# Optimization experiments

Measured on AMD Instinct MI355X. Metric: run time of the kernel, lower is better.

The kernel has to match this reference:

```python
import jax, jax.numpy as jnp
import numpy as np

N = 10000          # nodes
E = 80000          # edges
STATE_DIM = 18
HID = 1024
LAYERS = 4


def setup_inputs() -> dict:
    key = jax.random.key(0)
    ks = jax.random.split(key, 16)
    s = 0.02
    x = jax.random.normal(ks[0], (N, STATE_DIM), dtype=jnp.float32)
    edge_index = jax.random.randint(ks[1], (2, E), 0, N, dtype=jnp.int32)
    # frozen inverse-phase embedding projection (no bias)
    proj_w = jax.random.normal(ks[2], (STATE_DIM, HID), dtype=jnp.float32) * s
    # per-layer message MLP: Linear(2*HID -> HID) -> ReLU -> Linear(HID -> HID)
    W1 = jax.random.normal(ks[3], (LAYERS, 2 * HID, HID), dtype=jnp.float32) * s
    b1 = jnp.zeros((LAYERS, HID), dtype=jnp.float32)
    W2 = jax.random.normal(ks[4], (LAYERS, HID, HID), dtype=jnp.float32) * s
    b2 = jnp.zeros((LAYERS, HID), dtype=jnp.float32)
    # ghost head: Linear(HID->256) -> ReLU -> Linear(256->1) -> Sigmoid
    gw1 = jax.random.normal(ks[5], (HID, 256), dtype=jnp.float32) * s
    gb1 = jnp.zeros((256,), dtype=jnp.float32)
    gw2 = jax.random.normal(ks[6], (256, 1), dtype=jnp.float32) * s
    gb2 = jnp.zeros((1,), dtype=jnp.float32)
    # state head: Linear(HID -> STATE_DIM)
    sw = jax.random.normal(ks[7], (HID, STATE_DIM), dtype=jnp.float32) * s
    sb = jnp.zeros((STATE_DIM,), dtype=jnp.float32)
    return {"x": x, "edge_index": edge_index, "proj_w": proj_w,
            "W1": W1, "b1": b1, "W2": W2, "b2": b2,
            "gw1": gw1, "gb1": gb1, "gw2": gw2, "gb2": gb2,
            "sw": sw, "sb": sb}


def reference(x, edge_index, proj_w, W1, b1, W2, b2, gw1, gb1, gw2, gb2, sw, sb):
    src = edge_index[0]  # j (source)
    dst = edge_index[1]  # i (target), aggr='add' scatters into i
    # InversePhaseEmbedding: sin(h)*cos(h)
    p = x @ proj_w                      # [N, HID]
    h = jnp.sin(p) * jnp.cos(p)
    for l in range(LAYERS):
        x_i = h[dst]                    # [E, HID] gather target feats
        x_j = h[src]                    # [E, HID] gather source feats
        msg = jnp.concatenate([x_i, x_j - x_i], axis=-1)  # [E, 2*HID]
        m = jax.nn.relu(msg @ W1[l] + b1[l]) @ W2[l] + b2[l]  # [E, HID]
        h = jax.ops.segment_sum(m, dst, num_segments=N)       # scatter-add
        h = jax.nn.relu(h)
    ghost_score = jax.nn.sigmoid(jax.nn.relu(h @ gw1 + gb1) @ gw2 + gb2)  # [N,1]
    stable_state = h @ sw + sb                                            # [N,18]
    return ghost_score, stable_state, h
```

## Files before the change

kernel.cpp:

```cpp
#include <hip/hip_runtime.h>
#include <hip/hip_bf16.h>
#include <math.h>

#define NN 10000
#define EE 80000
#define SDIM 18
#define HID 1024
#define NLAYERS 4
#define GHID 256

typedef __bf16 bf16;
typedef __bf16 bf16x8 __attribute__((ext_vector_type(8)));
typedef __bf16 bf16x4 __attribute__((ext_vector_type(4)));
typedef float f32x4 __attribute__((ext_vector_type(4)));

#define AS1C(p) ((const __attribute__((address_space(1))) void*)(p))
#define AS3(p)  ((__attribute__((address_space(3))) void*)(p))

__global__ void count_kernel(const int* __restrict__ ei, int* __restrict__ cnt) {
    int e = blockIdx.x * 256 + threadIdx.x;
    if (e < EE) atomicAdd(&cnt[ei[EE + e]], 1);
}

__global__ __launch_bounds__(256) void scan_kernel(const int* __restrict__ cnt,
                                                   int* __restrict__ offs,
                                                   int* __restrict__ cursor,
                                                   float* __restrict__ degF) {
    const int CH = 40;
    __shared__ int partial[256];
    int t = threadIdx.x;
    int base = t * CH;
    int local[CH];
    int sum = 0;
#pragma unroll
    for (int i = 0; i < CH; ++i) {
        int idx = base + i;
        int v = (idx < NN) ? cnt[idx] : 0;
        local[i] = sum;
        sum += v;
    }
    partial[t] = sum;
    __syncthreads();
    for (int off = 1; off < 256; off <<= 1) {
        int v = (t >= off) ? partial[t - off] : 0;
        __syncthreads();
        partial[t] += v;
        __syncthreads();
    }
    int excl = (t == 0) ? 0 : partial[t - 1];
#pragma unroll
    for (int i = 0; i < CH; ++i) {
        int idx = base + i;
        if (idx < NN) {
            int o = excl + local[i];
            offs[idx] = o;
            cursor[idx] = o;
            degF[idx] = (float)cnt[idx];
        }
    }
    if (t == 255) offs[NN] = partial[255];
}

__global__ void scatter_kernel(const int* __restrict__ ei, int* __restrict__ cursor,
                               int* __restrict__ esrc) {
    int e = blockIdx.x * 256 + threadIdx.x;
    if (e < EE) {
        int dst = ei[EE + e];
        int pos = atomicAdd(&cursor[dst], 1);
        esrc[pos] = ei[e];
    }
}

__global__ __launch_bounds__(256) void prep_kernel(const float* __restrict__ W1,
                                                   const float* __restrict__ W2,
                                                   const float* __restrict__ gw1,
                                                   const float* __restrict__ sw,
                                                   const float* __restrict__ b1,
                                                   bf16* __restrict__ WT,
                                                   bf16* __restrict__ W2t,
                                                   bf16* __restrict__ gw1t,
                                                   bf16* __restrict__ swt,
                                                   float* __restrict__ cb,
                                                   int* __restrict__ cnt) {
    __shared__ float td[32][33];
    __shared__ float tb[32][33];
    const size_t H2 = (size_t)HID * HID;
    int b = blockIdx.x;
    int tx = threadIdx.x & 31, ty = threadIdx.x >> 5;

    if (b < 4096) {
        int l = b >> 10, r = b & 1023;
        int bx = (r & 31) * 32, by = (r >> 5) * 32;
        const float* s = W1 + (size_t)l * 2 * H2;
        bf16* d = WT + (size_t)l * 2 * H2;
#pragma unroll
        for (int r4 = 0; r4 < 4; ++r4) {
            int row = by + ty + r4 * 8;
            float vt = s[(size_t)row * HID + bx + tx];
            float vb = s[H2 + (size_t)row * HID + bx + tx];
            td[ty + r4 * 8][tx] = vt - vb;
            tb[ty + r4 * 8][tx] = vb;
        }
        __syncthreads();
#pragma unroll
        for (int r4 = 0; r4 < 4; ++r4) {
            int orow = bx + ty + r4 * 8;
            d[(size_t)orow * HID + by + tx] = (bf16)td[tx][ty + r4 * 8];
            d[(size_t)(HID + orow) * HID + by + tx] = (bf16)tb[tx][ty + r4 * 8];
        }
    } else if (b < 8192) {
        int sub = b - 4096;
        int l = sub >> 10, r = sub & 1023;
        int bx = (r & 31) * 32, by = (r >> 5) * 32;
        const float* s = W2 + (size_t)l * H2;
        bf16* d = W2t + (size_t)l * H2;
#pragma unroll
        for (int r4 = 0; r4 < 4; ++r4) {
            int row = by + ty + r4 * 8;
            td[ty + r4 * 8][tx] = s[(size_t)row * HID + bx + tx];
        }
        __syncthreads();
#pragma unroll
        for (int r4 = 0; r4 < 4; ++r4) {
            int orow = bx + ty + r4 * 8;
            d[(size_t)orow * HID + by + tx] = (bf16)td[tx][ty + r4 * 8];
        }
    } else if (b < 8448) {
        int sub = b - 8192;
        int bx = (sub & 7) * 32, by = (sub >> 3) * 32;
#pragma unroll
        for (int r4 = 0; r4 < 4; ++r4) {
            int row = by + ty + r4 * 8;
            td[ty + r4 * 8][tx] = gw1[(size_t)row * GHID + bx + tx];
        }
        __syncthreads();
#pragma unroll
        for (int r4 = 0; r4 < 4; ++r4) {
            int orow = bx + ty + r4 * 8;
            gw1t[(size_t)orow * HID + by + tx] = (bf16)td[tx][ty + r4 * 8];
        }
    } else if (b < 8576) {
        int i = (b - 8448) * 256 + threadIdx.x;
        int n = i >> 10, k = i & 1023;
        swt[i] = (bf16)(n < SDIM ? sw[k * SDIM + n] : 0.f);
    } else if (b < 8608) {
        int i = (b - 8576) * 256 + threadIdx.x;
        int l = i >> 11, c = i & 2047;
        cb[i] = (c < HID) ? b1[l * HID + c] : 0.f;
    } else {
        int i = (b - 8608) * 256 + threadIdx.x;
        if (i < NN) cnt[i] = 0;
    }
}

__global__ __launch_bounds__(256) void proj_kernel(const float* __restrict__ x,
                                                   const float* __restrict__ pw,
                                                   bf16* __restrict__ hb) {
    int row = blockIdx.y;
    int col = blockIdx.x * 256 + threadIdx.x;
    __shared__ float xr[SDIM];
    if (threadIdx.x < SDIM) xr[threadIdx.x] = x[row * SDIM + threadIdx.x];
    __syncthreads();
    float acc = 0.f;
#pragma unroll
    for (int k = 0; k < SDIM; ++k) acc += xr[k] * pw[k * HID + col];
    hb[(size_t)row * HID + col] = (bf16)(sinf(acc) * cosf(acc));
}

template <int RELU, int HAS_BIAS, int HAS_RS, int WF32, int WB16>
__global__ __launch_bounds__(256) void mgemm_kernel(const bf16* __restrict__ A,
                                                    const bf16* __restrict__ Bt,
                                                    float* __restrict__ C,
                                                    bf16* __restrict__ Cb,
                                                    const float* __restrict__ bias,
                                                    const float* __restrict__ rowscale,
                                                    int M, int N, int K) {
    __shared__ bf16 As[2][128 * 32];
    __shared__ bf16 Bs[2][128 * 32];
    const int tid = threadIdx.x;

    const int num_n = gridDim.x, num_m = gridDim.y;
    int bid = blockIdx.x + blockIdx.y * num_n;
    const int GROUP = 8;
    int width = GROUP * num_n;
    int group = bid / width;
    int rem = bid - group * width;
    int rows_ing = num_m - group * GROUP;
    rows_ing = rows_ing < GROUP ? rows_ing : GROUP;
    int by = group * GROUP + rem % rows_ing;
    int bx = rem / rows_ing;
    const int m0 = by * 128;
    const int n0 = bx * 128;

    const int wave = tid >> 6;
    const int wr = (wave >> 1) * 64, wc = (wave & 1) * 64;
    const int lane = tid & 63;
    const int quad = lane >> 4, r15 = lane & 15;

    f32x4 acc[4][4] = {};

    const int s0 = tid, s1 = 256 + tid;
    const int seg0 = ((s0 & 3) ^ ((s0 >> 3) & 3)) * 8;
    const int seg1 = ((s1 & 3) ^ ((s1 >> 3) & 3)) * 8;
    int ar0 = m0 + (s0 >> 2); ar0 = ar0 < M ? ar0 : M - 1;
    int ar1 = m0 + (s1 >> 2); ar1 = ar1 < M ? ar1 : M - 1;
    const bf16* ga0 = A + (size_t)ar0 * K + seg0;
    const bf16* ga1 = A + (size_t)ar1 * K + seg1;
    const bf16* gb0 = Bt + (size_t)(n0 + (s0 >> 2)) * K + seg0;
    const bf16* gb1 = Bt + (size_t)(n0 + (s1 >> 2)) * K + seg1;
    const int lofs0 = (tid & ~63) * 8;
    const int lofs1 = 2048 + (tid & ~63) * 8;

    int aoff[4], boff[4];
#pragma unroll
    for (int i = 0; i < 4; ++i) {
        int rA = wr + i * 16 + r15;
        aoff[i] = rA * 32 + (quad ^ ((rA >> 1) & 3)) * 8;
        int rB = wc + i * 16 + r15;
        boff[i] = rB * 32 + (quad ^ ((rB >> 1) & 3)) * 8;
    }

    __builtin_amdgcn_global_load_lds(AS1C(ga0), AS3(&As[0][lofs0]), 16, 0, 0);
    __builtin_amdgcn_global_load_lds(AS1C(ga1), AS3(&As[0][lofs1]), 16, 0, 0);
    __builtin_amdgcn_global_load_lds(AS1C(gb0), AS3(&Bs[0][lofs0]), 16, 0, 0);
    __builtin_amdgcn_global_load_lds(AS1C(gb1), AS3(&Bs[0][lofs1]), 16, 0, 0);

    const int NIT = K >> 5;
    for (int k = 0; k < NIT; ++k) {
        const int buf = k & 1;
        __syncthreads();
        if (k + 1 < NIT) {
            const int ko = (k + 1) << 5;
            __builtin_amdgcn_global_load_lds(AS1C(ga0 + ko), AS3(&As[buf ^ 1][lofs0]), 16, 0, 0);
            __builtin_amdgcn_global_load_lds(AS1C(ga1 + ko), AS3(&As[buf ^ 1][lofs1]), 16, 0, 0);
            __builtin_amdgcn_global_load_lds(AS1C(gb0 + ko), AS3(&Bs[buf ^ 1][lofs0]), 16, 0, 0);
            __builtin_amdgcn_global_load_lds(AS1C(gb1 + ko), AS3(&Bs[buf ^ 1][lofs1]), 16, 0, 0);
        }
        bf16x8 af[4], bfr[4];
#pragma unroll
        for (int i = 0; i < 4; ++i)
            af[i] = *(const bf16x8*)(&As[buf][aoff[i]]);
#pragma unroll
        for (int j = 0; j < 4; ++j)
            bfr[j] = *(const bf16x8*)(&Bs[buf][boff[j]]);
#pragma unroll
        for (int i = 0; i < 4; ++i)
#pragma unroll
            for (int j = 0; j < 4; ++j)
                acc[i][j] = __builtin_amdgcn_mfma_f32_16x16x32_bf16(af[i], bfr[j], acc[i][j], 0, 0, 0);
    }

#pragma unroll
    for (int i = 0; i < 4; ++i) {
#pragma unroll
        for (int r = 0; r < 4; ++r) {
            int grow = m0 + wr + i * 16 + quad * 4 + r;
            if (grow >= M) continue;
            float rs = HAS_RS ? rowscale[grow] : 1.f;
#pragma unroll
            for (int j = 0; j < 4; ++j) {
                int gcol = n0 + wc + j * 16 + r15;
                float v = acc[i][j][r];
                if (HAS_BIAS) v += rs * bias[gcol];
                if (RELU) v = fmaxf(v, 0.f);
                if (WF32) C[(size_t)grow * N + gcol] = v;
                if (WB16) Cb[(size_t)grow * N + gcol] = (bf16)v;
            }
        }
    }
}

__global__ __launch_bounds__(256) void gather_kernel(const int* __restrict__ offs,
                                                     const int* __restrict__ esrc,
                                                     const bf16* __restrict__ CB,
                                                     bf16* __restrict__ Sb) {
    int half = threadIdx.x >> 7;
    int t = threadIdx.x & 127;
    int node = blockIdx.x * 2 + half;
    int c = t * 8;
    int k0 = offs[node], k1 = offs[node + 1];
    bf16x8 cv = *(const bf16x8*)(CB + (size_t)node * 2048 + c);
    float cf[8], a[8];
#pragma unroll
    for (int i = 0; i < 8; ++i) { cf[i] = (float)cv[i]; a[i] = 0.f; }
    for (int k = k0; k < k1; ++k) {
        int s = esrc[k];
        bf16x8 bv = *(const bf16x8*)(CB + (size_t)s * 2048 + 1024 + c);
#pragma unroll
        for (int i = 0; i < 8; ++i) a[i] += fmaxf(cf[i] + (float)bv[i], 0.f);
    }
    bf16x8 o;
#pragma unroll
    for (int i = 0; i < 8; ++i) o[i] = (bf16)a[i];
    *(bf16x8*)(Sb + (size_t)node * HID + c) = o;
}

__global__ __launch_bounds__(64) void stable_mfma_kernel(const bf16* __restrict__ hb,
                                                         const bf16* __restrict__ swt,
                                                         const float* __restrict__ sb,
                                                         float* __restrict__ out) {
    int m0 = blockIdx.x * 16;
    int lane = threadIdx.x;
    int quad = lane >> 4, r15 = lane & 15;
    f32x4 acc0 = {}, acc1 = {};
    const bf16* arow = hb + (size_t)(m0 + r15) * HID + quad * 8;
    const bf16* b0 = swt + (size_t)r15 * HID + quad * 8;
    const bf16* b1p = swt + (size_t)(16 + r15) * HID + quad * 8;
    for (int k0 = 0; k0 < HID; k0 += 32) {
        bf16x8 af = *(const bf16x8*)(arow + k0);
        bf16x8 bf0 = *(const bf16x8*)(b0 + k0);
        bf16x8 bf1 = *(const bf16x8*)(b1p + k0);
        acc0 = __builtin_amdgcn_mfma_f32_16x16x32_bf16(af, bf0, acc0, 0, 0, 0);
        acc1 = __builtin_amdgcn_mfma_f32_16x16x32_bf16(af, bf1, acc1, 0, 0, 0);
    }
#pragma unroll
    for (int r = 0; r < 4; ++r) {
        int grow = m0 + quad * 4 + r;
        out[(size_t)grow * SDIM + r15] = acc0[r] + sb[r15];
        if (r15 < 2) out[(size_t)grow * SDIM + 16 + r15] = acc1[r] + sb[16 + r15];
    }
}

__global__ __launch_bounds__(256) void ghost_kernel(const float* __restrict__ g1,
                                                    const float* __restrict__ gw2,
                                                    const float* __restrict__ gb2,
                                                    float* __restrict__ out) {
    int w = threadIdx.x >> 6, lane = threadIdx.x & 63;
    int row = blockIdx.x * 4 + w;
    const float4 gv = *(const float4*)(g1 + (size_t)row * GHID + lane * 4);
    const float4 wv = *(const float4*)(gw2 + lane * 4);
    float v = gv.x * wv.x + gv.y * wv.y + gv.z * wv.z + gv.w * wv.w;
#pragma unroll
    for (int o = 32; o > 0; o >>= 1) v += __shfl_down(v, o, 64);
    if (lane == 0) out[row] = 1.f / (1.f + expf(-(v + gb2[0])));
}

extern "C" void kernel_launch(void* const* d_in, const int* in_sizes, int n_in,
                              void* d_out, int out_size, void* d_ws, size_t ws_size,
                              hipStream_t stream) {
    const float* x   = (const float*)d_in[0];
    const int*   ei  = (const int*)d_in[1];
    const float* pw  = (const float*)d_in[2];
    const float* W1  = (const float*)d_in[3];
    const float* b1  = (const float*)d_in[4];
    const float* W2  = (const float*)d_in[5];
    const float* b2  = (const float*)d_in[6];
    const float* gw1 = (const float*)d_in[7];
    const float* gb1 = (const float*)d_in[8];
    const float* gw2 = (const float*)d_in[9];
    const float* gb2 = (const float*)d_in[10];
    const float* sw  = (const float*)d_in[11];
    const float* sb  = (const float*)d_in[12];

    float* out    = (float*)d_out;
    float* ghost  = out;
    float* stable = out + NN;
    float* h      = out + NN + NN * SDIM;

    const size_t H2 = (size_t)HID * HID;
    float* ws   = (float*)d_ws;
    float* g1   = ws;
    float* degF = g1 + (size_t)NN * GHID;
    float* cb   = degF + NN;
    bf16* hb    = (bf16*)(cb + 4 * 2048);
    bf16* Sb    = hb + (size_t)NN * HID;
    bf16* CB    = Sb + (size_t)NN * HID;
    bf16* WT    = CB + (size_t)NN * 2048;
    bf16* W2t   = WT + 8 * H2;
    bf16* gw1t  = W2t + 4 * H2;
    bf16* swt   = gw1t + (size_t)GHID * HID;
    int*  cnt    = (int*)(swt + 32 * 1024);
    int*  offs   = cnt + NN;
    int*  cursor = offs + NN + 1;
    int*  esrc   = cursor + NN;

    prep_kernel<<<dim3(8648), 256, 0, stream>>>(W1, W2, gw1, sw, b1, WT, W2t, gw1t, swt, cb, cnt);

    count_kernel<<<dim3((EE + 255) / 256), 256, 0, stream>>>(ei, cnt);
    scan_kernel<<<dim3(1), 256, 0, stream>>>(cnt, offs, cursor, degF);
    scatter_kernel<<<dim3((EE + 255) / 256), 256, 0, stream>>>(ei, cursor, esrc);

    proj_kernel<<<dim3(HID / 256, NN), 256, 0, stream>>>(x, pw, hb);

    dim3 gfused(2048 / 128, (NN + 127) / 128);
    dim3 gw2g(HID / 128, (NN + 127) / 128);
    for (int l = 0; l < NLAYERS; ++l) {
        mgemm_kernel<0, 1, 0, 0, 1><<<gfused, 256, 0, stream>>>(
            hb, WT + (size_t)l * 2 * H2, nullptr, CB, cb + l * 2048, nullptr, NN, 2048, HID);
        gather_kernel<<<dim3(NN / 2), 256, 0, stream>>>(offs, esrc, CB, Sb);
        if (l < NLAYERS - 1)
            mgemm_kernel<1, 1, 1, 0, 1><<<gw2g, 256, 0, stream>>>(
                Sb, W2t + (size_t)l * H2, nullptr, hb, b2 + (size_t)l * HID, degF, NN, HID, HID);
        else
            mgemm_kernel<1, 1, 1, 1, 1><<<gw2g, 256, 0, stream>>>(
                Sb, W2t + (size_t)l * H2, h, hb, b2 + (size_t)l * HID, degF, NN, HID, HID);
    }

    mgemm_kernel<1, 1, 0, 1, 0><<<dim3(GHID / 128, (NN + 127) / 128), 256, 0, stream>>>(
        hb, gw1t, g1, nullptr, gb1, nullptr, NN, GHID, HID);
    ghost_kernel<<<dim3(NN / 4), 256, 0, stream>>>(g1, gw2, gb2, ghost);
    stable_mfma_kernel<<<dim3(NN / 16), 64, 0, stream>>>(hb, swt, sb, stable);
}
```

Baseline: 743.6 us.

## Add 256x128 triple-buffered MFMA GEMM with grouped tile ordering for layer GEMMs

Adds a new GEMM kernel for the per-layer node GEMMs. It uses 512-thread blocks with a 256x128 output tile, three-stage LDS buffering fed by direct global-to-LDS loads, and swizzled LDS offsets. Blocks are remapped in groups of 8 along M to improve L2 reuse, and MFMA issue is wrapped in raised wave priority. The larger tile raises data reuse per block but produces fewer blocks (about 40 along M) and needs 72KB of LDS, which may limit occupancy.

```diff
diff --git a/kernel.cpp b/kernel.cpp
--- a/kernel.cpp
+++ b/kernel.cpp
@@ -260,6 +260,114 @@
 #pragma unroll
             for (int j = 0; j < 4; ++j) {
                 int gcol = n0 + wc + j * 16 + r15;
+                float v = acc[i][j][r];
+                if (HAS_BIAS) v += rs * bias[gcol];
+                if (RELU) v = fmaxf(v, 0.f);
+                if (WF32) C[(size_t)grow * N + gcol] = v;
+                if (WB16) Cb[(size_t)grow * N + gcol] = (bf16)v;
+            }
+        }
+    }
+}
+
+template <int RELU, int HAS_BIAS, int HAS_RS, int WF32, int WB16>
+__global__ __launch_bounds__(512, 4) void mgemm3_kernel(const bf16* __restrict__ A,
+                                                        const bf16* __restrict__ Bt,
+                                                        float* __restrict__ C,
+                                                        bf16* __restrict__ Cb,
+                                                        const float* __restrict__ bias,
+                                                        const float* __restrict__ rowscale,
+                                                        int M, int N, int K) {
+    __shared__ bf16 lds[36864];
+    const int tid = threadIdx.x;
+    const int wave = tid >> 6, lane = tid & 63;
+    const int wm = wave >> 1, wn = wave & 1;
+    const int quad = lane >> 4, r15 = lane & 15;
+
+    const int num_n = gridDim.x, num_m = gridDim.y;
+    int bid = blockIdx.x + blockIdx.y * num_n;
+    const int GROUP = 8;
+    int width = GROUP * num_n;
+    int group = bid / width;
+    int rem = bid - group * width;
+    int rows_ing = num_m - group * GROUP;
+    rows_ing = rows_ing < GROUP ? rows_ing : GROUP;
+    int by = group * GROUP + rem % rows_ing;
+    int bx = rem / rows_ing;
+    const int m0 = by * 256, n0 = bx * 128;
+
+    const int strow = tid >> 2;
+    const int segsw = ((tid & 3) ^ ((tid >> 3) & 3)) * 8;
+    int ar0 = m0 + strow;        ar0 = ar0 < M ? ar0 : M - 1;
+    int ar1 = m0 + 128 + strow;  ar1 = ar1 < M ? ar1 : M - 1;
+    const bf16* ga0 = A + (size_t)ar0 * K + segsw;
+    const bf16* ga1 = A + (size_t)ar1 * K + segsw;
+    const bf16* gb  = Bt + (size_t)(n0 + strow) * K + segsw;
+    const int ldst = (tid & ~63) * 8;
+
+    int aoff[4], boff[4];
+#pragma unroll
+    for (int i = 0; i < 4; ++i) {
+        int rA = wm * 64 + i * 16 + r15;
+        aoff[i] = 12288 + rA * 32 + (quad ^ ((rA >> 1) & 3)) * 8;
+        int rB = wn * 64 + i * 16 + r15;
+        boff[i] = rB * 32 + (quad ^ ((rB >> 1) & 3)) * 8;
+    }
+
+    f32x4 acc[4][4] = {};
+
+#define STAGE3(bs, kt)                                                                                \
+    do {                                                                                              \
+        const int ko_ = (kt) << 5;                                                                    \
+        __builtin_amdgcn_global_load_lds(AS1C(ga0 + ko_), AS3(&lds[12288 + (bs)*8192 + ldst]), 16, 0, 0); \
+        __builtin_amdgcn_global_load_lds(AS1C(ga1 + ko_), AS3(&lds[12288 + (bs)*8192 + 4096 + ldst]), 16, 0, 0); \
+        __builtin_amdgcn_global_load_lds(AS1C(gb + ko_), AS3(&lds[(bs)*4096 + ldst]), 16, 0, 0);      \
+    } while (0)
+
+    STAGE3(0, 0);
+    STAGE3(1, 1);
+    asm volatile("s_waitcnt vmcnt(3)");
+    __builtin_amdgcn_s_barrier();
+
+    const int NT = K >> 5;
+    int t = 0;
+
+#define TILE3(bi, bs)                                                                          \
+    do {                                                                                       \
+        int kt = (t + 2 < NT) ? (t + 2) : (t - 1);  \
+        bf16x8 aF[4], bF[4];                                                                   \
+        _Pragma("unroll") for (int i = 0; i < 4; ++i)                                          \
+            aF[i] = *(const bf16x8*)(&lds[(bi)*8192 + aoff[i]]);                               \
+        _Pragma("unroll") for (int j = 0; j < 4; ++j)                                          \
+            bF[j] = *(const bf16x8*)(&lds[(bi)*4096 + boff[j]]);                               \
+        STAGE3(bs, kt);                                                                        \
+        asm volatile("s_waitcnt lgkmcnt(0)");                                                  \
+        __builtin_amdgcn_s_setprio(1);                                                         \
+        _Pragma("unroll") for (int i = 0; i < 4; ++i)                                          \
+            _Pragma("unroll") for (int j = 0; j < 4; ++j)                                      \
+                acc[i][j] = __builtin_amdgcn_mfma_f32_16x16x32_bf16(aF[i], bF[j], acc[i][j], 0, 0, 0); \
+        __builtin_amdgcn_s_setprio(0);                                                         \
+        asm volatile("s_waitcnt vmcnt(3)");          \
+        __builtin_amdgcn_s_barrier();                                                          \
+        ++t;                                                                                   \
+    } while (0)
+
+    while (t + 3 <= NT) { TILE3(0, 2); TILE3(1, 0); TILE3(2, 1); }
+    if (t < NT) TILE3(0, 2);
+    if (t < NT) TILE3(1, 0);
+#undef TILE3
+#undef STAGE3
+
+#pragma unroll
+    for (int i = 0; i < 4; ++i) {
+#pragma unroll
+        for (int r = 0; r < 4; ++r) {
+            int grow = m0 + wm * 64 + i * 16 + quad * 4 + r;
+            if (grow >= M) continue;
+            float rs = HAS_RS ? rowscale[grow] : 1.f;
+#pragma unroll
+            for (int j = 0; j < 4; ++j) {
+                int gcol = n0 + wn * 64 + j * 16 + r15;
                 float v = acc[i][j][r];
                 if (HAS_BIAS) v += rs * bias[gcol];
                 if (RELU) v = fmaxf(v, 0.f);
@@ -382,17 +490,17 @@
 
     proj_kernel<<<dim3(HID / 256, NN), 256, 0, stream>>>(x, pw, hb);
 
-    dim3 gfused(2048 / 128, (NN + 127) / 128);
-    dim3 gw2g(HID / 128, (NN + 127) / 128);
+    dim3 gcbg(2048 / 128, (NN + 255) / 256);
+    dim3 gw2grid(HID / 128, (NN + 255) / 256);
     for (int l = 0; l < NLAYERS; ++l) {
-        mgemm_kernel<0, 1, 0, 0, 1><<<gfused, 256, 0, stream>>>(
+        mgemm3_kernel<0, 1, 0, 0, 1><<<gcbg, 512, 0, stream>>>(
             hb, WT + (size_t)l * 2 * H2, nullptr, CB, cb + l * 2048, nullptr, NN, 2048, HID);
         gather_kernel<<<dim3(NN / 2), 256, 0, stream>>>(offs, esrc, CB, Sb);
         if (l < NLAYERS - 1)
-            mgemm_kernel<1, 1, 1, 0, 1><<<gw2g, 256, 0, stream>>>(
+            mgemm3_kernel<1, 1, 1, 0, 1><<<gw2grid, 512, 0, stream>>>(
                 Sb, W2t + (size_t)l * H2, nullptr, hb, b2 + (size_t)l * HID, degF, NN, HID, HID);
         else
-            mgemm_kernel<1, 1, 1, 1, 1><<<gw2g, 256, 0, stream>>>(
+            mgemm3_kernel<1, 1, 1, 1, 1><<<gw2grid, 512, 0, stream>>>(
                 Sb, W2t + (size_t)l * H2, h, hb, b2 + (size_t)l * HID, degF, NN, HID, HID);
     }
 
```

Result: faster. 720.7 us (-3.1%).
